# Kernel tuning notes

Measured on AMD Instinct MI355X. Metric: run time of the kernel, lower is better.

The kernel has to match this reference:

```python
import jax, jax.numpy as jnp
import numpy as np

NUM_HEADS = 16
EMBED_DIM = 1024
HEAD_DIM = EMBED_DIM // NUM_HEADS


def setup_inputs() -> dict:
    key = jax.random.key(0)
    ks = jax.random.split(key, 9)
    B, S, D = 4, 2048, EMBED_DIM
    scale = 1.0 / np.sqrt(D)
    inp = {
        "x": jax.random.normal(ks[0], (B, S, D), dtype=jnp.float32),
        "Wq": jax.random.normal(ks[1], (D, D), dtype=jnp.float32) * scale,
        "bq": jnp.zeros((D,), dtype=jnp.float32),
        "Wk": jax.random.normal(ks[2], (D, D), dtype=jnp.float32) * scale,
        "bk": jnp.zeros((D,), dtype=jnp.float32),
        "Wv": jax.random.normal(ks[3], (D, D), dtype=jnp.float32) * scale,
        "bv": jnp.zeros((D,), dtype=jnp.float32),
        "Wo": jax.random.normal(ks[4], (D, D), dtype=jnp.float32) * scale,
        "bo": jnp.zeros((D,), dtype=jnp.float32),
    }
    return inp


def reference(x, Wq, bq, Wk, bk, Wv, bv, Wo, bo):
    # x: [B, S, D]; weights stored torch-style as [out, in] -> use x @ W.T + b
    B, S, D = x.shape
    H, Hd = NUM_HEADS, HEAD_DIM

    def proj(W, b):
        return (jnp.einsum('bsd,ed->bse', x, W) + b).reshape(B, S, H, Hd).transpose(0, 2, 1, 3)

    Q = proj(Wq, bq)  # [B, H, S, Hd]
    K = proj(Wk, bk)
    V = proj(Wv, bv)

    scores = jnp.einsum('bhqd,bhkd->bhqk', Q, K) / jnp.sqrt(jnp.float32(Hd))
    attn = jax.nn.softmax(scores, axis=-1)  # dropout is identity in eval mode
    context = jnp.einsum('bhqk,bhkd->bhqd', attn, V)
    context = context.transpose(0, 2, 1, 3).reshape(B, S, D)
    out = jnp.einsum('bsd,ed->bse', context, Wo) + bo
    return out
```

## Files before the change

kernel.cpp:

```cpp
#include <hip/hip_runtime.h>


#define LOG2E 1.4426950408889634f
#define QSCALE (0.125f * LOG2E)

typedef __bf16 bf16x8 __attribute__((ext_vector_type(8)));
typedef float f32x4 __attribute__((ext_vector_type(4)));
typedef unsigned short u16x4 __attribute__((ext_vector_type(4)));
typedef unsigned short u16x8 __attribute__((ext_vector_type(8)));
typedef unsigned int u32x4 __attribute__((ext_vector_type(4)));

__device__ __forceinline__ unsigned short f2bf(float f) {
  unsigned int u = __builtin_bit_cast(unsigned int, f);
  u += 0x7fffu + ((u >> 16) & 1u);
  return (unsigned short)(u >> 16);
}

__device__ __forceinline__ unsigned int pack2bf(float a, float b) {
  unsigned int ua = __builtin_bit_cast(unsigned int, a);
  unsigned int ub = __builtin_bit_cast(unsigned int, b);
  ua += 0x7fffu + ((ua >> 16) & 1u);
  ub += 0x7fffu + ((ub >> 16) & 1u);
  return __builtin_amdgcn_perm(ub, ua, 0x07060302u);
}

typedef const __attribute__((address_space(1))) void* gptr_t;
typedef __attribute__((address_space(3))) void* lptr_t;
__device__ __forceinline__ void gload16(const void* g, void* l) {
  __builtin_amdgcn_global_load_lds((gptr_t)g, (lptr_t)l, 16, 0, 0);
}

__global__ __launch_bounds__(256) void k_cvt(const float* __restrict__ x,
                                             const float* __restrict__ Wq, const float* __restrict__ Wk,
                                             const float* __restrict__ Wv, const float* __restrict__ Wo,
                                             unsigned short* __restrict__ xb, unsigned short* __restrict__ Wb) {
  int gi = (blockIdx.x * 256 + threadIdx.x) * 4;
  if (gi < 8388608) {
    f32x4 v = *(const f32x4*)(x + gi);
    u16x4 o; o[0] = f2bf(v[0]); o[1] = f2bf(v[1]); o[2] = f2bf(v[2]); o[3] = f2bf(v[3]);
    *(u16x4*)(xb + gi) = o;
  } else {
    int i = gi - 8388608;
    int wsel = i >> 20;
    int loc = i & 1048575;
    const float* src = (wsel == 0) ? Wq : (wsel == 1) ? Wk : (wsel == 2) ? Wv : Wo;
    float sc = (wsel == 0) ? QSCALE : 1.0f;
    f32x4 v = *(const f32x4*)(src + loc);
    u16x4 o; o[0] = f2bf(v[0] * sc); o[1] = f2bf(v[1] * sc); o[2] = f2bf(v[2] * sc); o[3] = f2bf(v[3] * sc);
    *(u16x4*)(Wb + i) = o;
  }
}

__global__ __launch_bounds__(256, 2) void k_gemm_qkv(
    const unsigned short* __restrict__ xb, const unsigned short* __restrict__ Wb,
    const float* __restrict__ bq, const float* __restrict__ bk, const float* __restrict__ bv,
    unsigned short* __restrict__ Qb, unsigned short* __restrict__ Kb, unsigned short* __restrict__ Vtb) {
  __shared__ unsigned short As[128 * 32];
  __shared__ unsigned short Bs[128 * 32];
  const int tid = threadIdx.x;
  const int lane = tid & 63;
  const int w = tid >> 6;
  const int wm = w & 1;
  const int wn = w >> 1;
  const int z = blockIdx.z;
  const int m0 = blockIdx.y * 128;
  const int n0 = blockIdx.x * 128;
  const unsigned short* W = Wb + ((size_t)z << 20);

  const int srow = tid >> 2;
  const int sch = (tid & 3) << 3;
  const size_t a0 = (size_t)(m0 + srow) * 1024 + sch;
  const size_t b0 = (size_t)(n0 + srow) * 1024 + sch;

  f32x4 zero4 = {0.f, 0.f, 0.f, 0.f};
  f32x4 acc[4][4];
#pragma unroll
  for (int i = 0; i < 4; ++i)
#pragma unroll
    for (int jj = 0; jj < 4; ++jj) acc[i][jj] = zero4;

  const int fr = lane & 15;
  const int fk = (lane >> 4) << 3;

  for (int kt = 0; kt < 32; ++kt) {
    const int ko = kt << 5;
    __syncthreads();
    gload16(xb + a0 + ko, As + tid * 8);
    gload16(xb + a0 + (size_t)65536 + ko, As + 2048 + tid * 8);
    gload16(W + b0 + ko, Bs + tid * 8);
    gload16(W + b0 + (size_t)65536 + ko, Bs + 2048 + tid * 8);
    __syncthreads();
    bf16x8 af[4], bfr[4];
#pragma unroll
    for (int mt = 0; mt < 4; ++mt)
      af[mt] = *(const bf16x8*)&As[(wm * 64 + mt * 16 + fr) * 32 + fk];
#pragma unroll
    for (int nt = 0; nt < 4; ++nt)
      bfr[nt] = *(const bf16x8*)&Bs[(wn * 64 + nt * 16 + fr) * 32 + fk];
#pragma unroll
    for (int mt = 0; mt < 4; ++mt)
#pragma unroll
      for (int nt = 0; nt < 4; ++nt)
        acc[mt][nt] = __builtin_amdgcn_mfma_f32_16x16x32_bf16(af[mt], bfr[nt], acc[mt][nt], 0, 0, 0);
  }

  const float* bias = (z == 0) ? bq : (z == 1) ? bk : bv;
  const float bsc = (z == 0) ? QSCALE : 1.0f;
  const int rg = (lane >> 4) << 2;
#pragma unroll
  for (int mt = 0; mt < 4; ++mt) {
    const int mb = m0 + wm * 64 + mt * 16 + rg;
    const int b = mb >> 11;
    const int s = mb & 2047;
#pragma unroll
    for (int nt = 0; nt < 4; ++nt) {
      const int n = n0 + wn * 64 + nt * 16 + fr;
      const float bvv = bias[n] * bsc;
      const int h = n >> 6;
      const int d = n & 63;
      if (z == 2) {
        u16x4 pk;
#pragma unroll
        for (int r = 0; r < 4; ++r) pk[r] = f2bf(acc[mt][nt][r] + bvv);
        const int pbase = (s & ~31) | ((s & 12) << 1) | ((s & 16) >> 2);
        *(u16x4*)&Vtb[(((size_t)(b * 16 + h) << 6) + d) * 2048 + pbase] = pk;
      } else {
        unsigned short* O = (z == 0) ? Qb : Kb;
#pragma unroll
        for (int r = 0; r < 4; ++r)
          O[(((size_t)(b * 16 + h) << 11) + s + r) * 64 + d] = f2bf(acc[mt][nt][r] + bvv);
      }
    }
  }
}

__global__ __launch_bounds__(256, 3) void k_flash(
    const unsigned short* __restrict__ Qb, const unsigned short* __restrict__ Kb,
    const unsigned short* __restrict__ Vtb, unsigned short* __restrict__ Ctx) {
  __shared__ unsigned short Ks[2 * 128 * 64];
  __shared__ unsigned short Vts[64 * 128];
  const int tid = threadIdx.x;
  const int lane = tid & 63;
  const int wq = tid >> 6;
  const int fr = lane & 15;
  const int qd = lane >> 4;
  const int bh = blockIdx.y;
  const int q0 = blockIdx.x << 7;
  const size_t hoff = (size_t)bh << 17;
  const unsigned short* Qh = Qb + hoff + ((size_t)q0 << 6);

  const unsigned short* kg[4];
  const unsigned short* vg[4];
  unsigned short* kl[4];
  unsigned short* vl[4];
#pragma unroll
  for (int p = 0; p < 4; ++p) {
    int slot = p * 256 + tid;
    int kr = slot >> 3, ch = slot & 7;
    kg[p] = Kb + hoff + (size_t)kr * 64 + ((ch ^ (kr & 7)) << 3);
    kl[p] = Ks + slot * 8;
    int dr = slot >> 4, ch2 = slot & 15;
    vg[p] = Vtb + hoff + (size_t)dr * 2048 + ((ch2 ^ (dr & 15)) << 3);
    vl[p] = Vts + slot * 8;
  }

  int kbase[2];
#pragma unroll
  for (int ds = 0; ds < 2; ++ds)
    kbase[ds] = fr * 64 + (((ds * 4 + qd) ^ (fr & 7)) << 3);
  int vbase[4];
#pragma unroll
  for (int ks = 0; ks < 4; ++ks)
    vbase[ks] = fr * 128 + (((ks * 4 + qd) ^ fr) << 3);

  bf16x8 qf[2][2];
#pragma unroll
  for (int qt = 0; qt < 2; ++qt)
#pragma unroll
    for (int ds = 0; ds < 2; ++ds)
      qf[qt][ds] = *(const bf16x8*)&Qh[(wq * 32 + qt * 16 + fr) * 64 + ds * 32 + qd * 8];

  f32x4 zero4 = {0.f, 0.f, 0.f, 0.f};
  f32x4 o_acc[2][4];
  float l_p[2] = {0.f, 0.f};
#pragma unroll
  for (int mt = 0; mt < 2; ++mt)
#pragma unroll
    for (int dt = 0; dt < 4; ++dt) o_acc[mt][dt] = zero4;

#pragma unroll
  for (int p = 0; p < 4; ++p) gload16(kg[p], kl[p]);
#pragma unroll
  for (int p = 0; p < 4; ++p) kg[p] += 128 * 64;
  __syncthreads();

  int curoff = 0;
  for (int j = 0; j < 16; ++j) {
#pragma unroll
    for (int p = 0; p < 4; ++p) gload16(vg[p], vl[p]);
#pragma unroll
    for (int p = 0; p < 4; ++p) gload16(kg[p], kl[p] + (curoff ^ 8192));
#pragma unroll
    for (int p = 0; p < 4; ++p) { kg[p] += 128 * 64; vg[p] += 128; }

    const unsigned short* Kc = Ks + curoff;
    u32x4 pfw[2][4];
#pragma unroll
    for (int ks = 0; ks < 4; ++ks) {
      f32x4 st0[2], st1[2];
      st0[0] = zero4; st0[1] = zero4; st1[0] = zero4; st1[1] = zero4;
#pragma unroll
      for (int ds = 0; ds < 2; ++ds) {
        bf16x8 kf0 = *(const bf16x8*)&Kc[kbase[ds] + (2 * ks) * 1024];
        bf16x8 kf1 = *(const bf16x8*)&Kc[kbase[ds] + (2 * ks + 1) * 1024];
        st0[0] = __builtin_amdgcn_mfma_f32_16x16x32_bf16(kf0, qf[0][ds], st0[0], 0, 0, 0);
        st0[1] = __builtin_amdgcn_mfma_f32_16x16x32_bf16(kf0, qf[1][ds], st0[1], 0, 0, 0);
        st1[0] = __builtin_amdgcn_mfma_f32_16x16x32_bf16(kf1, qf[0][ds], st1[0], 0, 0, 0);
        st1[1] = __builtin_amdgcn_mfma_f32_16x16x32_bf16(kf1, qf[1][ds], st1[1], 0, 0, 0);
      }
#pragma unroll
      for (int mt = 0; mt < 2; ++mt) {
#pragma unroll
        for (int r = 0; r < 4; ++r) {
          st0[mt][r] = __builtin_amdgcn_exp2f(st0[mt][r]);
          st1[mt][r] = __builtin_amdgcn_exp2f(st1[mt][r]);
        }
        l_p[mt] += ((st0[mt][0] + st0[mt][1]) + (st0[mt][2] + st0[mt][3])) +
                   ((st1[mt][0] + st1[mt][1]) + (st1[mt][2] + st1[mt][3]));
        u32x4 pk;
        pk[0] = pack2bf(st0[mt][0], st0[mt][1]);
        pk[1] = pack2bf(st0[mt][2], st0[mt][3]);
        pk[2] = pack2bf(st1[mt][0], st1[mt][1]);
        pk[3] = pack2bf(st1[mt][2], st1[mt][3]);
        pfw[mt][ks] = pk;
      }
    }

    asm volatile("s_waitcnt vmcnt(4)" ::: "memory");
    __builtin_amdgcn_s_barrier();

#pragma unroll
    for (int ks = 0; ks < 4; ++ks) {
      bf16x8 pf0 = __builtin_bit_cast(bf16x8, pfw[0][ks]);
      bf16x8 pf1 = __builtin_bit_cast(bf16x8, pfw[1][ks]);
#pragma unroll
      for (int dt = 0; dt < 4; ++dt) {
        bf16x8 vf = *(const bf16x8*)&Vts[vbase[ks] + dt * 2048];
        o_acc[0][dt] = __builtin_amdgcn_mfma_f32_16x16x32_bf16(pf0, vf, o_acc[0][dt], 0, 0, 0);
        o_acc[1][dt] = __builtin_amdgcn_mfma_f32_16x16x32_bf16(pf1, vf, o_acc[1][dt], 0, 0, 0);
      }
    }

    asm volatile("s_waitcnt vmcnt(0)" ::: "memory");
    __builtin_amdgcn_s_barrier();
    curoff ^= 8192;
  }

  float l_red[2];
#pragma unroll
  for (int mt = 0; mt < 2; ++mt) {
    float lv = l_p[mt];
    lv += __shfl_xor(lv, 16);
    lv += __shfl_xor(lv, 32);
    l_red[mt] = lv;
  }

  const int b = bh >> 4;
  const int h = bh & 15;
#pragma unroll
  for (int mt = 0; mt < 2; ++mt) {
#pragma unroll
    for (int r = 0; r < 4; ++r) {
      float lv = __shfl(l_red[mt], qd * 4 + r);
      float rl = 1.0f / lv;
      int s = q0 + wq * 32 + mt * 16 + qd * 4 + r;
      size_t base = (((size_t)b * 2048 + s) << 10) + (h << 6);
#pragma unroll
      for (int dt = 0; dt < 4; ++dt) Ctx[base + dt * 16 + fr] = f2bf(o_acc[mt][dt][r] * rl);
    }
  }
}

__global__ __launch_bounds__(256, 2) void k_gemm_out(
    const unsigned short* __restrict__ Ctx, const unsigned short* __restrict__ Wo,
    const float* __restrict__ bo, float* __restrict__ out) {
  __shared__ unsigned short As[128 * 32];
  __shared__ unsigned short Bs[128 * 32];
  const int tid = threadIdx.x;
  const int lane = tid & 63;
  const int w = tid >> 6;
  const int wm = w & 1;
  const int wn = w >> 1;
  const int m0 = blockIdx.y * 128;
  const int n0 = blockIdx.x * 128;

  const int srow = tid >> 2;
  const int sch = (tid & 3) << 3;
  const size_t a0 = (size_t)(m0 + srow) * 1024 + sch;
  const size_t b0 = (size_t)(n0 + srow) * 1024 + sch;

  f32x4 zero4 = {0.f, 0.f, 0.f, 0.f};
  f32x4 acc[4][4];
#pragma unroll
  for (int i = 0; i < 4; ++i)
#pragma unroll
    for (int jj = 0; jj < 4; ++jj) acc[i][jj] = zero4;

  const int fr = lane & 15;
  const int fk = (lane >> 4) << 3;

  for (int kt = 0; kt < 32; ++kt) {
    const int ko = kt << 5;
    __syncthreads();
    gload16(Ctx + a0 + ko, As + tid * 8);
    gload16(Ctx + a0 + (size_t)65536 + ko, As + 2048 + tid * 8);
    gload16(Wo + b0 + ko, Bs + tid * 8);
    gload16(Wo + b0 + (size_t)65536 + ko, Bs + 2048 + tid * 8);
    __syncthreads();
    bf16x8 af[4], bfr[4];
#pragma unroll
    for (int mt = 0; mt < 4; ++mt)
      af[mt] = *(const bf16x8*)&As[(wm * 64 + mt * 16 + fr) * 32 + fk];
#pragma unroll
    for (int nt = 0; nt < 4; ++nt)
      bfr[nt] = *(const bf16x8*)&Bs[(wn * 64 + nt * 16 + fr) * 32 + fk];
#pragma unroll
    for (int mt = 0; mt < 4; ++mt)
#pragma unroll
      for (int nt = 0; nt < 4; ++nt)
        acc[mt][nt] = __builtin_amdgcn_mfma_f32_16x16x32_bf16(af[mt], bfr[nt], acc[mt][nt], 0, 0, 0);
  }

  const int rg = (lane >> 4) << 2;
#pragma unroll
  for (int mt = 0; mt < 4; ++mt) {
    const int mb = m0 + wm * 64 + mt * 16 + rg;
#pragma unroll
    for (int nt = 0; nt < 4; ++nt) {
      const int n = n0 + wn * 64 + nt * 16 + fr;
      const float bvv = bo[n];
#pragma unroll
      for (int r = 0; r < 4; ++r)
        out[(size_t)(mb + r) * 1024 + n] = acc[mt][nt][r] + bvv;
    }
  }
}

extern "C" void kernel_launch(void* const* d_in, const int* in_sizes, int n_in,
                              void* d_out, int out_size, void* d_ws, size_t ws_size,
                              hipStream_t stream) {
  (void)in_sizes; (void)n_in; (void)out_size; (void)ws_size;
  const float* x = (const float*)d_in[0];
  const float* Wq = (const float*)d_in[1];
  const float* bq = (const float*)d_in[2];
  const float* Wk = (const float*)d_in[3];
  const float* bk = (const float*)d_in[4];
  const float* Wv = (const float*)d_in[5];
  const float* bv = (const float*)d_in[6];
  const float* Wo = (const float*)d_in[7];
  const float* bo = (const float*)d_in[8];
  float* out = (float*)d_out;

  unsigned short* xb = (unsigned short*)d_ws;
  unsigned short* Wb = xb + 8388608;
  unsigned short* Qb = Wb + 4194304;
  unsigned short* Kb = Qb + 8388608;
  unsigned short* Vtb = Kb + 8388608;
  unsigned short* Ctx = xb;

  k_cvt<<<12288, 256, 0, stream>>>(x, Wq, Wk, Wv, Wo, xb, Wb);
  k_gemm_qkv<<<dim3(8, 64, 3), 256, 0, stream>>>(xb, Wb, bq, bk, bv, Qb, Kb, Vtb);
  k_flash<<<dim3(16, 64), 256, 0, stream>>>(Qb, Kb, Vtb, Ctx);
  k_gemm_out<<<dim3(8, 64), 256, 0, stream>>>(Ctx, Wb + 3 * 1048576, bo, out);
}
```

Baseline: 288.7 us.

## Swizzle block order for XCD locality and use packed bf16 conversion in flash

```diff
diff --git a/kernel.cpp b/kernel.cpp
--- a/kernel.cpp
+++ b/kernel.cpp
@@ -6,6 +6,7 @@
 
 typedef __bf16 bf16x8 __attribute__((ext_vector_type(8)));
 typedef float f32x4 __attribute__((ext_vector_type(4)));
+typedef float f32x2 __attribute__((ext_vector_type(2)));
 typedef unsigned short u16x4 __attribute__((ext_vector_type(4)));
 typedef unsigned short u16x8 __attribute__((ext_vector_type(8)));
 typedef unsigned int u32x4 __attribute__((ext_vector_type(4)));
@@ -16,12 +17,10 @@
   return (unsigned short)(u >> 16);
 }
 
-__device__ __forceinline__ unsigned int pack2bf(float a, float b) {
-  unsigned int ua = __builtin_bit_cast(unsigned int, a);
-  unsigned int ub = __builtin_bit_cast(unsigned int, b);
-  ua += 0x7fffu + ((ua >> 16) & 1u);
-  ub += 0x7fffu + ((ub >> 16) & 1u);
-  return __builtin_amdgcn_perm(ub, ua, 0x07060302u);
+__device__ __forceinline__ unsigned int cvtpk(float a, float b) {
+  unsigned int r;
+  asm("v_cvt_pk_bf16_f32 %0, %1, %2" : "=v"(r) : "v"(a), "v"(b));
+  return r;
 }
 
 typedef const __attribute__((address_space(1))) void* gptr_t;
@@ -62,9 +61,11 @@
   const int w = tid >> 6;
   const int wm = w & 1;
   const int wn = w >> 1;
-  const int z = blockIdx.z;
-  const int m0 = blockIdx.y * 128;
-  const int n0 = blockIdx.x * 128;
+  const int lin = blockIdx.x + (blockIdx.y << 3) + (blockIdx.z << 9);
+  const int swz = (lin & 7) * 192 + (lin >> 3);
+  const int z = swz >> 9;
+  const int m0 = ((swz >> 3) & 63) << 7;
+  const int n0 = (swz & 7) << 7;
   const unsigned short* W = Wb + ((size_t)z << 20);
 
   const int srow = tid >> 2;
@@ -144,8 +145,10 @@
   const int wq = tid >> 6;
   const int fr = lane & 15;
   const int qd = lane >> 4;
-  const int bh = blockIdx.y;
-  const int q0 = blockIdx.x << 7;
+  const int lin = blockIdx.x + (blockIdx.y << 4);
+  const int swz = ((lin & 7) << 7) + (lin >> 3);
+  const int bh = swz >> 4;
+  const int q0 = (swz & 15) << 7;
   const size_t hoff = (size_t)bh << 17;
   const unsigned short* Qh = Qb + hoff + ((size_t)q0 << 6);
 
@@ -182,7 +185,7 @@
 
   f32x4 zero4 = {0.f, 0.f, 0.f, 0.f};
   f32x4 o_acc[2][4];
-  float l_p[2] = {0.f, 0.f};
+  f32x2 l2[2] = {{0.f, 0.f}, {0.f, 0.f}};
 #pragma unroll
   for (int mt = 0; mt < 2; ++mt)
 #pragma unroll
@@ -225,13 +228,16 @@
           st0[mt][r] = __builtin_amdgcn_exp2f(st0[mt][r]);
           st1[mt][r] = __builtin_amdgcn_exp2f(st1[mt][r]);
         }
-        l_p[mt] += ((st0[mt][0] + st0[mt][1]) + (st0[mt][2] + st0[mt][3])) +
-                   ((st1[mt][0] + st1[mt][1]) + (st1[mt][2] + st1[mt][3]));
+        f32x2 s01 = {st0[mt][0], st0[mt][1]};
+        f32x2 s23 = {st0[mt][2], st0[mt][3]};
+        f32x2 t01 = {st1[mt][0], st1[mt][1]};
+        f32x2 t23 = {st1[mt][2], st1[mt][3]};
+        l2[mt] += (s01 + s23) + (t01 + t23);
         u32x4 pk;
-        pk[0] = pack2bf(st0[mt][0], st0[mt][1]);
-        pk[1] = pack2bf(st0[mt][2], st0[mt][3]);
-        pk[2] = pack2bf(st1[mt][0], st1[mt][1]);
-        pk[3] = pack2bf(st1[mt][2], st1[mt][3]);
+        pk[0] = cvtpk(st0[mt][0], st0[mt][1]);
+        pk[1] = cvtpk(st0[mt][2], st0[mt][3]);
+        pk[2] = cvtpk(st1[mt][0], st1[mt][1]);
+        pk[3] = cvtpk(st1[mt][2], st1[mt][3]);
         pfw[mt][ks] = pk;
       }
     }
@@ -259,7 +265,7 @@
   float l_red[2];
 #pragma unroll
   for (int mt = 0; mt < 2; ++mt) {
-    float lv = l_p[mt];
+    float lv = l2[mt][0] + l2[mt][1];
     lv += __shfl_xor(lv, 16);
     lv += __shfl_xor(lv, 32);
     l_red[mt] = lv;
@@ -291,8 +297,10 @@
   const int w = tid >> 6;
   const int wm = w & 1;
   const int wn = w >> 1;
-  const int m0 = blockIdx.y * 128;
-  const int n0 = blockIdx.x * 128;
+  const int lin = blockIdx.x + (blockIdx.y << 3);
+  const int swz = ((lin & 7) << 6) + (lin >> 3);
+  const int m0 = (swz >> 3) << 7;
+  const int n0 = (swz & 7) << 7;
 
   const int srow = tid >> 2;
   const int sch = (tid & 3) << 3;
```

Result: faster. 273.3 us (-5.3%).
